# Kernel optimization log

Hardware: AMD Instinct MI355X
Metric: run time of the kernel (lower is better)

Reference implementation:

```python
import jax, jax.numpy as jnp
import numpy as np

N = 100_000   # nodes
E = 3_200_000 # edges
K = 3         # num_stacks
T = 4         # num_layers (shared weights)
H = 16        # hidden channels of conv1
EPS = 1e-5    # BatchNorm eps


def setup_inputs() -> dict:
    key = jax.random.key(0)
    ks = jax.random.split(key, 12)
    def glorot(k, shape):
        fan = shape[-2] + shape[-1]
        return jax.random.normal(k, shape, jnp.float32) * (2.0 / fan) ** 0.5
    return {
        "x": jax.random.normal(ks[0], (N, 1), jnp.float32),
        "edge_index": jax.random.randint(ks[1], (2, E), 0, N, jnp.int32),
        "edge_weight": jax.random.uniform(ks[2], (E,), jnp.float32),
        # conv1: in=1, out=16  (init_weight [K,Fin,Fout], shared weight [K,Fout,Fout], root [K,Fin,Fout], bias [K,Fout])
        "conv1_init_w": glorot(ks[3], (K, 1, H)),
        "conv1_w": glorot(ks[4], (K, H, H)),
        "conv1_root_w": glorot(ks[5], (K, 1, H)),
        "conv1_bias": jnp.zeros((K, H), jnp.float32),
        # BatchNorm1d(16) in eval mode: running stats + affine params
        "bn1_gamma": jnp.ones((H,), jnp.float32),
        "bn1_beta": jnp.zeros((H,), jnp.float32),
        "bn1_mean": jnp.zeros((H,), jnp.float32),
        "bn1_var": jnp.ones((H,), jnp.float32),
        # conv2: in=16, out=1, act=None
        "conv2_init_w": glorot(ks[6], (K, H, 1)),
        "conv2_w": glorot(ks[7], (K, 1, 1)),
        "conv2_root_w": glorot(ks[8], (K, H, 1)),
        "conv2_bias": jnp.zeros((K, 1), jnp.float32),
    }


def _gcn_norm(edge_index, edge_weight):
    # ARMAConv uses gcn_norm with add_self_loops=False
    row, col = edge_index[0], edge_index[1]
    deg = jax.ops.segment_sum(edge_weight, col, num_segments=N)
    dis = jnp.where(deg > 0, jax.lax.rsqrt(jnp.maximum(deg, 1e-12)), 0.0)
    norm = dis[row] * edge_weight * dis[col]
    return row, col, norm


def _arma(x, row, col, norm, init_w, w, root_w, bias, act):
    # x: [N, Fin]; out per stack: [K, N, Fout]
    root = jnp.einsum('nf,kfo->kno', x, root_w) + bias[:, None, :]
    out = jnp.einsum('nf,kfo->kno', x, init_w)
    for t in range(T):
        if t > 0:
            out = jnp.einsum('kno,kop->knp', out, w)  # shared weight
        msg = out[:, row, :] * norm[None, :, None]     # [K, E, F] gather + scale
        out = jax.ops.segment_sum(msg.transpose(1, 0, 2), col, num_segments=N)  # [N, K, F]
        out = out.transpose(1, 0, 2) + root            # scatter-add + skip (root)
        if act:
            out = jax.nn.relu(out)
    return out.mean(axis=0)  # mean over stacks -> [N, Fout]


def reference(x, edge_index, edge_weight,
              conv1_init_w, conv1_w, conv1_root_w, conv1_bias,
              bn1_gamma, bn1_beta, bn1_mean, bn1_var,
              conv2_init_w, conv2_w, conv2_root_w, conv2_bias):
    row, col, norm = _gcn_norm(edge_index, edge_weight)
    h = _arma(x, row, col, norm, conv1_init_w, conv1_w, conv1_root_w, conv1_bias, act=True)
    # BatchNorm1d (eval) + ReLU; dropout is identity in eval
    h = (h - bn1_mean) * jax.lax.rsqrt(bn1_var + EPS) * bn1_gamma + bn1_beta
    h = jax.nn.relu(h)
    h = _arma(h, row, col, norm, conv2_init_w, conv2_w, conv2_root_w, conv2_bias, act=False)
    return jax.nn.sigmoid(h)  # [N, 1]
```

## Files before the change

### kernel.cpp

```cpp
#include <hip/hip_runtime.h>
#include <math.h>

#define NN 100000
#define NE 3200000
#define NB 782
#define BCAP 4608
#define BN_EPS 1e-5f

static inline size_t alignup(size_t v) { return (v + 255) & ~size_t(255); }

__device__ inline unsigned short f2bf(float x) {
  unsigned u = __float_as_uint(x);
  u += 0x7FFF + ((u >> 16) & 1);
  return (unsigned short)(u >> 16);
}
__device__ inline float bf2f(unsigned short h) {
  return __uint_as_float((unsigned)h << 16);
}

__global__ void k_bin(const int* __restrict__ row, const int* __restrict__ col,
                      const float* __restrict__ ew, int* __restrict__ gfill,
                      int2* __restrict__ bin) {
  __shared__ int cnt[NB];
  __shared__ int base[NB];
  for (int i = threadIdx.x; i < NB; i += 256) cnt[i] = 0;
  __syncthreads();
  int e0 = blockIdx.x * 8192;
  for (int i = 0; i < 32; ++i) {
    int e = e0 + i * 256 + threadIdx.x;
    if (e < NE) atomicAdd(&cnt[col[e] >> 7], 1);
  }
  __syncthreads();
  for (int i = threadIdx.x; i < NB; i += 256) {
    int c = cnt[i];
    base[i] = (c > 0) ? atomicAdd(&gfill[i], c) : 0;
    cnt[i] = 0;
  }
  __syncthreads();
  for (int i = 0; i < 32; ++i) {
    int e = e0 + i * 256 + threadIdx.x;
    if (e < NE) {
      int c = col[e], b = c >> 7;
      int pos = base[b] + atomicAdd(&cnt[b], 1);
      if (pos < BCAP)
        bin[(size_t)b * BCAP + pos] =
            make_int2(row[e] | ((c & 127) << 17), __float_as_int(ew[e]));
    }
  }
}

__global__ void k_build(const int* __restrict__ gfill, int2* __restrict__ bin,
                        int* __restrict__ csr, float* __restrict__ dis,
                        int* __restrict__ nstart, int* __restrict__ ncnt) {
  __shared__ int2 stage[BCAP];
  __shared__ int cnt[128];
  __shared__ float degw[128];
  __shared__ int off[129];
  int b = blockIdx.x;
  int nb = min(gfill[b], BCAP);
  const int2* gb = bin + (size_t)b * BCAP;
  for (int i = threadIdx.x; i < 128; i += 256) { cnt[i] = 0; degw[i] = 0.f; }
  __syncthreads();
  for (int i = threadIdx.x; i < nb; i += 256) {
    int2 v = gb[i];
    stage[i] = v;
    int c = (v.x >> 17) & 127;
    atomicAdd(&cnt[c], 1);
    atomicAdd(&degw[c], __int_as_float(v.y));
  }
  __syncthreads();
  if (threadIdx.x == 0) {
    int s = 0;
    for (int c = 0; c < 128; ++c) { off[c] = s; s += cnt[c]; }
    off[128] = s;
  }
  __syncthreads();
  int gbase = b * BCAP;
  for (int c = threadIdx.x; c < 128; c += 256) {
    int n = b * 128 + c;
    if (n < NN) {
      nstart[n] = gbase + off[c];
      ncnt[n] = cnt[c];
      float d = degw[c];
      dis[n] = (d > 0.f) ? rsqrtf(fmaxf(d, 1e-12f)) : 0.f;
    }
  }
  __syncthreads();
  for (int i = threadIdx.x; i < 128; i += 256) cnt[i] = 0;
  __syncthreads();
  int* cb = csr + (size_t)b * BCAP;
  for (int i = threadIdx.x; i < nb; i += 256) {
    int2 v = stage[i];
    int c = (v.x >> 17) & 127;
    int pos = off[c] + atomicAdd(&cnt[c], 1);
    float w = __int_as_float(v.y);
    int q = (int)fminf(fmaf(w, 32767.f, 0.5f), 32767.f);
    cb[pos] = (v.x & 0x1FFFF) | (q << 17);
  }
}

__global__ void k_init1(const float* __restrict__ x, const float* __restrict__ rw,
                        const float* __restrict__ bias, const float* __restrict__ iw,
                        const float* __restrict__ dis,
                        float* __restrict__ root1, ushort4* __restrict__ buf0) {
  int idx = blockIdx.x * 256 + threadIdx.x;
  if (idx >= NN * 16) return;
  int n = idx >> 4, f = idx & 15;
  float xv = x[n], dn = dis[n];
  ushort4 pk;
  pk.x = f2bf(dn * xv * iw[f]);
  pk.y = f2bf(dn * xv * iw[16 + f]);
  pk.z = f2bf(dn * xv * iw[32 + f]);
  pk.w = 0;
  buf0[(size_t)n * 16 + f] = pk;
  root1[n * 48 + f]      = xv * rw[f]      + bias[f];
  root1[n * 48 + 16 + f] = xv * rw[16 + f] + bias[16 + f];
  root1[n * 48 + 32 + f] = xv * rw[32 + f] + bias[32 + f];
}

template <bool APPLY_W>
__global__ void k_prop16(const ushort4* __restrict__ in, const float* __restrict__ root,
                         ushort4* __restrict__ outp, const int* __restrict__ csr,
                         const int* __restrict__ nstart, const int* __restrict__ ncnt,
                         const float* __restrict__ dis, const float* __restrict__ w,
                         const float* __restrict__ bng, const float* __restrict__ bnb,
                         const float* __restrict__ bnm, const float* __restrict__ bnv,
                         const float* __restrict__ iw2, const float* __restrict__ rw2,
                         const float* __restrict__ b2,
                         float4* __restrict__ root2, float4* __restrict__ o2) {
  __shared__ float ws[768];
  if (APPLY_W) {
    for (int i = threadIdx.x; i < 768; i += 256) ws[i] = w[i];
    __syncthreads();
  }
  int f = threadIdx.x & 15;
  int n = (blockIdx.x * 256 + threadIdx.x) >> 4;
  if (n >= NN) return;
  int e0 = nstart[n], cnt = ncnt[n];
  float a0 = 0.f, a1 = 0.f, a2 = 0.f;
  int i = 0;
  for (; i + 4 <= cnt; i += 4) {
    int ea = csr[e0 + i];
    int eb = csr[e0 + i + 1];
    int ec = csr[e0 + i + 2];
    int ed = csr[e0 + i + 3];
    ushort4 va = in[(size_t)(ea & 0x1FFFF) * 16 + f];
    ushort4 vb = in[(size_t)(eb & 0x1FFFF) * 16 + f];
    ushort4 vc = in[(size_t)(ec & 0x1FFFF) * 16 + f];
    ushort4 vd = in[(size_t)(ed & 0x1FFFF) * 16 + f];
    float wa = (float)((unsigned)ea >> 17) * (1.f / 32767.f);
    float wb = (float)((unsigned)eb >> 17) * (1.f / 32767.f);
    float wc = (float)((unsigned)ec >> 17) * (1.f / 32767.f);
    float wd = (float)((unsigned)ed >> 17) * (1.f / 32767.f);
    a0 = fmaf(wa, bf2f(va.x), a0); a1 = fmaf(wa, bf2f(va.y), a1); a2 = fmaf(wa, bf2f(va.z), a2);
    a0 = fmaf(wb, bf2f(vb.x), a0); a1 = fmaf(wb, bf2f(vb.y), a1); a2 = fmaf(wb, bf2f(vb.z), a2);
    a0 = fmaf(wc, bf2f(vc.x), a0); a1 = fmaf(wc, bf2f(vc.y), a1); a2 = fmaf(wc, bf2f(vc.z), a2);
    a0 = fmaf(wd, bf2f(vd.x), a0); a1 = fmaf(wd, bf2f(vd.y), a1); a2 = fmaf(wd, bf2f(vd.z), a2);
  }
  for (; i < cnt; ++i) {
    int e = csr[e0 + i];
    float we = (float)((unsigned)e >> 17) * (1.f / 32767.f);
    ushort4 v = in[(size_t)(e & 0x1FFFF) * 16 + f];
    a0 = fmaf(we, bf2f(v.x), a0);
    a1 = fmaf(we, bf2f(v.y), a1);
    a2 = fmaf(we, bf2f(v.z), a2);
  }
  float dn = dis[n];
  a0 = fmaxf(fmaf(dn, a0, root[n * 48 + f]), 0.f);
  a1 = fmaxf(fmaf(dn, a1, root[n * 48 + 16 + f]), 0.f);
  a2 = fmaxf(fmaf(dn, a2, root[n * 48 + 32 + f]), 0.f);
  if (APPLY_W) {
    float n0 = 0.f, n1 = 0.f, n2 = 0.f;
    #pragma unroll
    for (int f2 = 0; f2 < 16; ++f2) {
      float b0 = __shfl(a0, f2, 16);
      float b1 = __shfl(a1, f2, 16);
      float b2v = __shfl(a2, f2, 16);
      n0 = fmaf(b0, ws[f2 * 16 + f], n0);
      n1 = fmaf(b1, ws[256 + f2 * 16 + f], n1);
      n2 = fmaf(b2v, ws[512 + f2 * 16 + f], n2);
    }
    ushort4 pk;
    pk.x = f2bf(dn * n0); pk.y = f2bf(dn * n1); pk.z = f2bf(dn * n2); pk.w = 0;
    outp[(size_t)n * 16 + f] = pk;
  } else {
    float mean = (a0 + a1 + a2) * (1.f / 3.f);
    float hv = fmaxf((mean - bnm[f]) * rsqrtf(bnv[f] + BN_EPS) * bng[f] + bnb[f], 0.f);
    float d0 = hv * iw2[f],      r0 = hv * rw2[f];
    float d1 = hv * iw2[16 + f], r1 = hv * rw2[16 + f];
    float d2 = hv * iw2[32 + f], r2 = hv * rw2[32 + f];
    #pragma unroll
    for (int d = 8; d; d >>= 1) {
      d0 += __shfl_xor(d0, d, 16); r0 += __shfl_xor(r0, d, 16);
      d1 += __shfl_xor(d1, d, 16); r1 += __shfl_xor(r1, d, 16);
      d2 += __shfl_xor(d2, d, 16); r2 += __shfl_xor(r2, d, 16);
    }
    if (f == 0) {
      float4 rt, oo;
      rt.x = r0 + b2[0]; rt.y = r1 + b2[1]; rt.z = r2 + b2[2]; rt.w = 0.f;
      oo.x = dn * d0; oo.y = dn * d1; oo.z = dn * d2; oo.w = 0.f;
      root2[n] = rt;
      o2[n] = oo;
    }
  }
}

template <bool LAST>
__global__ void k_prop1(const float4* __restrict__ in, const float4* __restrict__ root,
                        float4* __restrict__ outp, float* __restrict__ outf,
                        const int* __restrict__ csr,
                        const int* __restrict__ nstart, const int* __restrict__ ncnt,
                        const float* __restrict__ dis, const float* __restrict__ w2) {
  int lane = threadIdx.x & 15;
  int n = (blockIdx.x * 256 + threadIdx.x) >> 4;
  if (n >= NN) return;
  int e0 = nstart[n], cnt = ncnt[n];
  float a0 = 0.f, a1 = 0.f, a2 = 0.f;
  for (int i = lane; i < cnt; i += 16) {
    int e = csr[e0 + i];
    float we = (float)((unsigned)e >> 17) * (1.f / 32767.f);
    float4 src = in[e & 0x1FFFF];
    a0 = fmaf(we, src.x, a0);
    a1 = fmaf(we, src.y, a1);
    a2 = fmaf(we, src.z, a2);
  }
  #pragma unroll
  for (int d = 8; d; d >>= 1) {
    a0 += __shfl_xor(a0, d, 16);
    a1 += __shfl_xor(a1, d, 16);
    a2 += __shfl_xor(a2, d, 16);
  }
  if (lane == 0) {
    float dn = dis[n];
    float4 rt = root[n];
    if (LAST) {
      float s = fmaf(dn, a0, rt.x) + fmaf(dn, a1, rt.y) + fmaf(dn, a2, rt.z);
      s *= (1.f / 3.f);
      outf[n] = 1.f / (1.f + expf(-s));
    } else {
      float4 oo;
      oo.x = dn * fmaf(dn, a0, rt.x) * w2[0];
      oo.y = dn * fmaf(dn, a1, rt.y) * w2[1];
      oo.z = dn * fmaf(dn, a2, rt.z) * w2[2];
      oo.w = 0.f;
      outp[n] = oo;
    }
  }
}

extern "C" void kernel_launch(void* const* d_in, const int* in_sizes, int n_in,
                              void* d_out, int out_size, void* d_ws, size_t ws_size,
                              hipStream_t stream) {
  const float* x     = (const float*)d_in[0];
  const int*   ei    = (const int*)d_in[1];
  const float* ew    = (const float*)d_in[2];
  const float* c1_iw = (const float*)d_in[3];
  const float* c1_w  = (const float*)d_in[4];
  const float* c1_rw = (const float*)d_in[5];
  const float* c1_b  = (const float*)d_in[6];
  const float* bn_g  = (const float*)d_in[7];
  const float* bn_b  = (const float*)d_in[8];
  const float* bn_m  = (const float*)d_in[9];
  const float* bn_v  = (const float*)d_in[10];
  const float* c2_iw = (const float*)d_in[11];
  const float* c2_w  = (const float*)d_in[12];
  const float* c2_rw = (const float*)d_in[13];
  const float* c2_b  = (const float*)d_in[14];
  float* out = (float*)d_out;

  char* p = (char*)d_ws;
  auto take = [&](size_t bytes) -> char* { char* r = p; p += alignup(bytes); return r; };
  int*     gfill = (int*)take((size_t)NB * 4);
  int2*    bin   = (int2*)take((size_t)NB * BCAP * 8);
  int*     csr   = (int*)take((size_t)NB * BCAP * 4);
  float*   dis   = (float*)take((size_t)NN * 4);
  int*     nst   = (int*)take((size_t)NN * 4);
  int*     ncn   = (int*)take((size_t)NN * 4);
  float*   root1 = (float*)take((size_t)NN * 48 * 4);
  ushort4* bufA  = (ushort4*)take((size_t)NN * 16 * 8);
  ushort4* bufB  = (ushort4*)take((size_t)NN * 16 * 8);
  float4*  root2 = (float4*)take((size_t)NN * 16);
  float4*  o2A   = (float4*)take((size_t)NN * 16);
  float4*  o2B   = (float4*)take((size_t)NN * 16);

  hipMemsetAsync(gfill, 0, (size_t)NB * 4, stream);

  const int* row = ei;
  const int* col = ei + NE;

  const int gBin = (NE + 8191) / 8192;
  const int gP   = (NN * 16 + 255) / 256;

  k_bin<<<gBin, 256, 0, stream>>>(row, col, ew, gfill, bin);
  k_build<<<NB, 256, 0, stream>>>(gfill, bin, csr, dis, nst, ncn);

  k_init1<<<gP, 256, 0, stream>>>(x, c1_rw, c1_b, c1_iw, dis, root1, bufA);
  k_prop16<true ><<<gP, 256, 0, stream>>>(bufA, root1, bufB, csr, nst, ncn, dis, c1_w,
      nullptr, nullptr, nullptr, nullptr, nullptr, nullptr, nullptr, nullptr, nullptr);
  k_prop16<true ><<<gP, 256, 0, stream>>>(bufB, root1, bufA, csr, nst, ncn, dis, c1_w,
      nullptr, nullptr, nullptr, nullptr, nullptr, nullptr, nullptr, nullptr, nullptr);
  k_prop16<true ><<<gP, 256, 0, stream>>>(bufA, root1, bufB, csr, nst, ncn, dis, c1_w,
      nullptr, nullptr, nullptr, nullptr, nullptr, nullptr, nullptr, nullptr, nullptr);
  k_prop16<false><<<gP, 256, 0, stream>>>(bufB, root1, nullptr, csr, nst, ncn, dis, nullptr,
      bn_g, bn_b, bn_m, bn_v, c2_iw, c2_rw, c2_b, root2, o2A);

  k_prop1<false><<<gP, 256, 0, stream>>>(o2A, root2, o2B, nullptr, csr, nst, ncn, dis, c2_w);
  k_prop1<false><<<gP, 256, 0, stream>>>(o2B, root2, o2A, nullptr, csr, nst, ncn, dis, c2_w);
  k_prop1<false><<<gP, 256, 0, stream>>>(o2A, root2, o2B, nullptr, csr, nst, ncn, dis, c2_w);
  k_prop1<true ><<<gP, 256, 0, stream>>>(o2B, root2, nullptr, out, csr, nst, ncn, dis, c2_w);
}
```

Baseline: 438.0 us.

## Propagate scalar input in first conv1 layer, deepen gather unroll, shrink bin blocks

The first conv1 propagation now aggregates a single scalar per node (dis*x) and applies the rank-1 init weight after aggregation, instead of gathering 48-wide bf16 features. This removes most of the gather traffic from one of the four 16-wide propagation passes. The gather loop is also unrolled to 8 edges to keep more loads in flight, k_bin uses smaller edge blocks to get more parallelism, and k_build drops its LDS staging buffer and rereads from global memory. The scalar path changes the rounding order slightly, and rereading the bin adds some global traffic.

```diff
diff --git a/kernel.cpp b/kernel.cpp
--- a/kernel.cpp
+++ b/kernel.cpp
@@ -5,6 +5,7 @@
 #define NE 3200000
 #define NB 782
 #define BCAP 4608
+#define EPB 2048
 #define BN_EPS 1e-5f
 
 static inline size_t alignup(size_t v) { return (v + 255) & ~size_t(255); }
@@ -25,11 +26,9 @@
   __shared__ int base[NB];
   for (int i = threadIdx.x; i < NB; i += 256) cnt[i] = 0;
   __syncthreads();
-  int e0 = blockIdx.x * 8192;
-  for (int i = 0; i < 32; ++i) {
-    int e = e0 + i * 256 + threadIdx.x;
-    if (e < NE) atomicAdd(&cnt[col[e] >> 7], 1);
-  }
+  int e0 = blockIdx.x * EPB;
+  int nE = min(EPB, NE - e0);
+  for (int i = threadIdx.x; i < nE; i += 256) atomicAdd(&cnt[col[e0 + i] >> 7], 1);
   __syncthreads();
   for (int i = threadIdx.x; i < NB; i += 256) {
     int c = cnt[i];
@@ -37,22 +36,19 @@
     cnt[i] = 0;
   }
   __syncthreads();
-  for (int i = 0; i < 32; ++i) {
-    int e = e0 + i * 256 + threadIdx.x;
-    if (e < NE) {
-      int c = col[e], b = c >> 7;
-      int pos = base[b] + atomicAdd(&cnt[b], 1);
-      if (pos < BCAP)
-        bin[(size_t)b * BCAP + pos] =
-            make_int2(row[e] | ((c & 127) << 17), __float_as_int(ew[e]));
-    }
-  }
-}
-
-__global__ void k_build(const int* __restrict__ gfill, int2* __restrict__ bin,
+  for (int i = threadIdx.x; i < nE; i += 256) {
+    int e = e0 + i;
+    int c = col[e], b = c >> 7;
+    int pos = base[b] + atomicAdd(&cnt[b], 1);
+    if (pos < BCAP)
+      bin[(size_t)b * BCAP + pos] =
+          make_int2(row[e] | ((c & 127) << 17), __float_as_int(ew[e]));
+  }
+}
+
+__global__ void k_build(const int* __restrict__ gfill, const int2* __restrict__ bin,
                         int* __restrict__ csr, float* __restrict__ dis,
                         int* __restrict__ nstart, int* __restrict__ ncnt) {
-  __shared__ int2 stage[BCAP];
   __shared__ int cnt[128];
   __shared__ float degw[128];
   __shared__ int off[129];
@@ -63,7 +59,6 @@
   __syncthreads();
   for (int i = threadIdx.x; i < nb; i += 256) {
     int2 v = gb[i];
-    stage[i] = v;
     int c = (v.x >> 17) & 127;
     atomicAdd(&cnt[c], 1);
     atomicAdd(&degw[c], __int_as_float(v.y));
@@ -90,7 +85,7 @@
   __syncthreads();
   int* cb = csr + (size_t)b * BCAP;
   for (int i = threadIdx.x; i < nb; i += 256) {
-    int2 v = stage[i];
+    int2 v = gb[i];
     int c = (v.x >> 17) & 127;
     int pos = off[c] + atomicAdd(&cnt[c], 1);
     float w = __int_as_float(v.y);
@@ -100,22 +95,56 @@
 }
 
 __global__ void k_init1(const float* __restrict__ x, const float* __restrict__ rw,
-                        const float* __restrict__ bias, const float* __restrict__ iw,
-                        const float* __restrict__ dis,
-                        float* __restrict__ root1, ushort4* __restrict__ buf0) {
+                        const float* __restrict__ bias, const float* __restrict__ dis,
+                        float* __restrict__ root1, float* __restrict__ s) {
   int idx = blockIdx.x * 256 + threadIdx.x;
   if (idx >= NN * 16) return;
   int n = idx >> 4, f = idx & 15;
-  float xv = x[n], dn = dis[n];
-  ushort4 pk;
-  pk.x = f2bf(dn * xv * iw[f]);
-  pk.y = f2bf(dn * xv * iw[16 + f]);
-  pk.z = f2bf(dn * xv * iw[32 + f]);
-  pk.w = 0;
-  buf0[(size_t)n * 16 + f] = pk;
+  float xv = x[n];
+  if (f == 0) s[n] = dis[n] * xv;
   root1[n * 48 + f]      = xv * rw[f]      + bias[f];
   root1[n * 48 + 16 + f] = xv * rw[16 + f] + bias[16 + f];
   root1[n * 48 + 32 + f] = xv * rw[32 + f] + bias[32 + f];
+}
+
+__global__ void k_prop_first(const float* __restrict__ s, const float* __restrict__ root,
+                             ushort4* __restrict__ outp, const int* __restrict__ csr,
+                             const int* __restrict__ nstart, const int* __restrict__ ncnt,
+                             const float* __restrict__ dis, const float* __restrict__ w,
+                             const float* __restrict__ iw) {
+  __shared__ float ws[768];
+  for (int i = threadIdx.x; i < 768; i += 256) ws[i] = w[i];
+  __syncthreads();
+  int f = threadIdx.x & 15;
+  int n = (blockIdx.x * 256 + threadIdx.x) >> 4;
+  if (n >= NN) return;
+  int e0 = nstart[n], cnt = ncnt[n];
+  float g = 0.f;
+  for (int i = f; i < cnt; i += 16) {
+    int e = csr[e0 + i];
+    float we = (float)((unsigned)e >> 17) * (1.f / 32767.f);
+    g = fmaf(we, s[e & 0x1FFFF], g);
+  }
+  #pragma unroll
+  for (int d = 8; d; d >>= 1) g += __shfl_xor(g, d, 16);
+  float dn = dis[n];
+  float dg = dn * g;
+  float a0 = fmaxf(fmaf(dg, iw[f],      root[n * 48 + f]),      0.f);
+  float a1 = fmaxf(fmaf(dg, iw[16 + f], root[n * 48 + 16 + f]), 0.f);
+  float a2 = fmaxf(fmaf(dg, iw[32 + f], root[n * 48 + 32 + f]), 0.f);
+  float n0 = 0.f, n1 = 0.f, n2 = 0.f;
+  #pragma unroll
+  for (int f2 = 0; f2 < 16; ++f2) {
+    float b0 = __shfl(a0, f2, 16);
+    float b1 = __shfl(a1, f2, 16);
+    float b2v = __shfl(a2, f2, 16);
+    n0 = fmaf(b0, ws[f2 * 16 + f], n0);
+    n1 = fmaf(b1, ws[256 + f2 * 16 + f], n1);
+    n2 = fmaf(b2v, ws[512 + f2 * 16 + f], n2);
+  }
+  ushort4 pk;
+  pk.x = f2bf(dn * n0); pk.y = f2bf(dn * n1); pk.z = f2bf(dn * n2); pk.w = 0;
+  outp[(size_t)n * 16 + f] = pk;
 }
 
 template <bool APPLY_W>
@@ -139,23 +168,35 @@
   int e0 = nstart[n], cnt = ncnt[n];
   float a0 = 0.f, a1 = 0.f, a2 = 0.f;
   int i = 0;
+  for (; i + 8 <= cnt; i += 8) {
+    int e[8];
+    ushort4 v[8];
+    #pragma unroll
+    for (int j = 0; j < 8; ++j) e[j] = csr[e0 + i + j];
+    #pragma unroll
+    for (int j = 0; j < 8; ++j) v[j] = in[(size_t)(e[j] & 0x1FFFF) * 16 + f];
+    #pragma unroll
+    for (int j = 0; j < 8; ++j) {
+      float we = (float)((unsigned)e[j] >> 17) * (1.f / 32767.f);
+      a0 = fmaf(we, bf2f(v[j].x), a0);
+      a1 = fmaf(we, bf2f(v[j].y), a1);
+      a2 = fmaf(we, bf2f(v[j].z), a2);
+    }
+  }
   for (; i + 4 <= cnt; i += 4) {
-    int ea = csr[e0 + i];
-    int eb = csr[e0 + i + 1];
-    int ec = csr[e0 + i + 2];
-    int ed = csr[e0 + i + 3];
-    ushort4 va = in[(size_t)(ea & 0x1FFFF) * 16 + f];
-    ushort4 vb = in[(size_t)(eb & 0x1FFFF) * 16 + f];
-    ushort4 vc = in[(size_t)(ec & 0x1FFFF) * 16 + f];
-    ushort4 vd = in[(size_t)(ed & 0x1FFFF) * 16 + f];
-    float wa = (float)((unsigned)ea >> 17) * (1.f / 32767.f);
-    float wb = (float)((unsigned)eb >> 17) * (1.f / 32767.f);
-    float wc = (float)((unsigned)ec >> 17) * (1.f / 32767.f);
-    float wd = (float)((unsigned)ed >> 17) * (1.f / 32767.f);
-    a0 = fmaf(wa, bf2f(va.x), a0); a1 = fmaf(wa, bf2f(va.y), a1); a2 = fmaf(wa, bf2f(va.z), a2);
-    a0 = fmaf(wb, bf2f(vb.x), a0); a1 = fmaf(wb, bf2f(vb.y), a1); a2 = fmaf(wb, bf2f(vb.z), a2);
-    a0 = fmaf(wc, bf2f(vc.x), a0); a1 = fmaf(wc, bf2f(vc.y), a1); a2 = fmaf(wc, bf2f(vc.z), a2);
-    a0 = fmaf(wd, bf2f(vd.x), a0); a1 = fmaf(wd, bf2f(vd.y), a1); a2 = fmaf(wd, bf2f(vd.z), a2);
+    int e[4];
+    ushort4 v[4];
+    #pragma unroll
+    for (int j = 0; j < 4; ++j) e[j] = csr[e0 + i + j];
+    #pragma unroll
+    for (int j = 0; j < 4; ++j) v[j] = in[(size_t)(e[j] & 0x1FFFF) * 16 + f];
+    #pragma unroll
+    for (int j = 0; j < 4; ++j) {
+      float we = (float)((unsigned)e[j] >> 17) * (1.f / 32767.f);
+      a0 = fmaf(we, bf2f(v[j].x), a0);
+      a1 = fmaf(we, bf2f(v[j].y), a1);
+      a2 = fmaf(we, bf2f(v[j].z), a2);
+    }
   }
   for (; i < cnt; ++i) {
     int e = csr[e0 + i];
@@ -277,6 +318,7 @@
   int*     nst   = (int*)take((size_t)NN * 4);
   int*     ncn   = (int*)take((size_t)NN * 4);
   float*   root1 = (float*)take((size_t)NN * 48 * 4);
+  float*   sbuf  = (float*)take((size_t)NN * 4);
   ushort4* bufA  = (ushort4*)take((size_t)NN * 16 * 8);
   ushort4* bufB  = (ushort4*)take((size_t)NN * 16 * 8);
   float4*  root2 = (float4*)take((size_t)NN * 16);
@@ -288,20 +330,19 @@
   const int* row = ei;
   const int* col = ei + NE;
 
-  const int gBin = (NE + 8191) / 8192;
+  const int gBin = (NE + EPB - 1) / EPB;
   const int gP   = (NN * 16 + 255) / 256;
 
   k_bin<<<gBin, 256, 0, stream>>>(row, col, ew, gfill, bin);
   k_build<<<NB, 256, 0, stream>>>(gfill, bin, csr, dis, nst, ncn);
 
-  k_init1<<<gP, 256, 0, stream>>>(x, c1_rw, c1_b, c1_iw, dis, root1, bufA);
+  k_init1<<<gP, 256, 0, stream>>>(x, c1_rw, c1_b, dis, root1, sbuf);
+  k_prop_first<<<gP, 256, 0, stream>>>(sbuf, root1, bufA, csr, nst, ncn, dis, c1_w, c1_iw);
   k_prop16<true ><<<gP, 256, 0, stream>>>(bufA, root1, bufB, csr, nst, ncn, dis, c1_w,
       nullptr, nullptr, nullptr, nullptr, nullptr, nullptr, nullptr, nullptr, nullptr);
   k_prop16<true ><<<gP, 256, 0, stream>>>(bufB, root1, bufA, csr, nst, ncn, dis, c1_w,
       nullptr, nullptr, nullptr, nullptr, nullptr, nullptr, nullptr, nullptr, nullptr);
-  k_prop16<true ><<<gP, 256, 0, stream>>>(bufA, root1, bufB, csr, nst, ncn, dis, c1_w,
-      nullptr, nullptr, nullptr, nullptr, nullptr, nullptr, nullptr, nullptr, nullptr);
-  k_prop16<false><<<gP, 256, 0, stream>>>(bufB, root1, nullptr, csr, nst, ncn, dis, nullptr,
+  k_prop16<false><<<gP, 256, 0, stream>>>(bufA, root1, nullptr, csr, nst, ncn, dis, nullptr,
       bn_g, bn_b, bn_m, bn_v, c2_iw, c2_rw, c2_b, root2, o2A);
 
   k_prop1<false><<<gP, 256, 0, stream>>>(o2A, root2, o2B, nullptr, csr, nst, ncn, dis, c2_w);
```

After: 416.1 us. -5.0%, faster.
